# Optimization experiments

Measured on AMD Instinct MI355X. Metric: run time of the kernel, lower is better.

Reference implementation:

```python
import jax, jax.numpy as jnp
import numpy as np

B, L, E = 512, 64, 1024
D_MODEL, H = 1024, 16
HD = D_MODEL // H  # 64
SMOL_CH, SMOL_HID, SMOL_GEN = 32, 256, 256
LN_EPS = 1e-3


def _layernorm(x, g, b, eps=LN_EPS):
    m = jnp.mean(x, axis=-1, keepdims=True)
    v = jnp.mean(jnp.square(x - m), axis=-1, keepdims=True)
    return (x - m) * jax.lax.rsqrt(v + eps) * g + b


def setup_inputs() -> dict:
    key = jax.random.key(0)
    ks = jax.random.split(key, 12)
    s = lambda fan_in: 1.0 / np.sqrt(fan_in)
    inp = {
        'x': jax.random.normal(ks[0], (B, L, E), dtype=jnp.float32),
        # attention projections (stored as [in, out])
        'wq': jax.random.normal(ks[1], (E, D_MODEL), dtype=jnp.float32) * s(E),
        'bq': jnp.zeros((D_MODEL,), jnp.float32),
        'wk': jax.random.normal(ks[2], (E, D_MODEL), dtype=jnp.float32) * s(E),
        'bk': jnp.zeros((D_MODEL,), jnp.float32),
        'wv': jax.random.normal(ks[3], (E, D_MODEL), dtype=jnp.float32) * s(E),
        'bv': jnp.zeros((D_MODEL,), jnp.float32),
        'wo': jax.random.normal(ks[4], (D_MODEL, E), dtype=jnp.float32) * s(D_MODEL),
        'bo': jnp.zeros((E,), jnp.float32),
        # smolgen hypernetwork
        'sc_w': jax.random.normal(ks[5], (E, SMOL_CH), dtype=jnp.float32) * s(E),
        'sh1_w': jax.random.normal(ks[6], (L * SMOL_CH, SMOL_HID), dtype=jnp.float32) * s(L * SMOL_CH),
        'sh1_b': jnp.zeros((SMOL_HID,), jnp.float32),
        'ln1_g': jnp.ones((SMOL_HID,), jnp.float32),
        'ln1_b': jnp.zeros((SMOL_HID,), jnp.float32),
        'sg_w': jax.random.normal(ks[7], (SMOL_HID, H * SMOL_GEN), dtype=jnp.float32) * s(SMOL_HID),
        'sg_b': jnp.zeros((H * SMOL_GEN,), jnp.float32),
        'ln2_g': jnp.ones((H * SMOL_GEN,), jnp.float32),
        'ln2_b': jnp.zeros((H * SMOL_GEN,), jnp.float32),
        'swg_w': jax.random.normal(ks[8], (SMOL_GEN, L * L), dtype=jnp.float32) * s(SMOL_GEN),
    }
    return inp


def reference(x, wq, bq, wk, bk, wv, bv, wo, bo,
              sc_w, sh1_w, sh1_b, ln1_g, ln1_b,
              sg_w, sg_b, ln2_g, ln2_b, swg_w):
    b, l, _ = x.shape
    # q/k/v projections -> [b, h, l, hd]
    q = (x @ wq + bq).reshape(b, l, H, HD).transpose(0, 2, 1, 3)
    k = (x @ wk + bk).reshape(b, l, H, HD).transpose(0, 2, 1, 3)
    v = (x @ wv + bv).reshape(b, l, H, HD).transpose(0, 2, 1, 3)

    scale = jnp.sqrt(jnp.asarray(HD, x.dtype))
    attn_logits = jnp.einsum('bhqd,bhkd->bhqk', q, k) / scale  # [b,h,l,l]

    # smolgen: per-batch, per-head additive bias on the logits
    compressed = (x @ sc_w).reshape(b, l * SMOL_CH)            # [b, 2048]
    hidden = _layernorm(jax.nn.silu(compressed @ sh1_w + sh1_b), ln1_g, ln1_b)
    gen = _layernorm(jax.nn.silu(hidden @ sg_w + sg_b), ln2_g, ln2_b)
    gen = gen.reshape(b, H, SMOL_GEN)
    smol_w = (gen @ swg_w).reshape(b, H, l, l)
    attn_logits = attn_logits + smol_w

    # manual numerically-stable softmax (as in source)
    attn_logits = attn_logits - jnp.max(attn_logits, axis=-1, keepdims=True)
    attn_weights = jnp.exp(attn_logits)
    attn_weights = attn_weights / jnp.sum(attn_weights, axis=-1, keepdims=True)

    attn_output = jnp.einsum('bhqk,bhkd->bhqd', attn_weights, v)
    attn_output = attn_output.transpose(0, 2, 1, 3).reshape(b, l, D_MODEL)
    return attn_output @ wo + bo
```

## Files before the change

### kernel.cpp

```cpp
#include <hip/hip_runtime.h>
#include <hip/hip_bf16.h>

typedef unsigned short u16;
typedef __attribute__((ext_vector_type(8))) short short8;
typedef __attribute__((ext_vector_type(4))) float f32x4;
typedef const __attribute__((address_space(1))) void GV;
typedef __attribute__((address_space(3))) void LV;
#define GLOAD16(g, l) __builtin_amdgcn_global_load_lds((GV*)(g), (LV*)(l), 16, 0, 0)
#define BAR() asm volatile("s_barrier" ::: "memory")

#define BATCH 512
#define LSEQ  64
#define EMB   1024
#define NH    16
#define NQKV  3328
#define MROWS (BATCH*LSEQ)

__device__ __forceinline__ u16 f2b(float f){
  __hip_bfloat16 h = __float2bfloat16(f);
  return *reinterpret_cast<u16*>(&h);
}
__device__ __forceinline__ float b2f(u16 u){
  return __uint_as_float(((unsigned)u) << 16);
}

__global__ __launch_bounds__(256) void f32_to_bf16_v4(const float* __restrict__ src,
                                                      u16* __restrict__ dst){
  size_t i = ((size_t)blockIdx.x * 256 + threadIdx.x) * 4;
  float4 v = *(const float4*)&src[i];
  unsigned lo = (unsigned)f2b(v.x) | ((unsigned)f2b(v.y) << 16);
  unsigned hi = (unsigned)f2b(v.z) | ((unsigned)f2b(v.w) << 16);
  *(uint2*)&dst[i] = make_uint2(lo, hi);
}

__global__ __launch_bounds__(256) void transpose_to_bf16(const float* __restrict__ src,
                                                         u16* __restrict__ dst,
                                                         int K, int N, int dstLd, int dstRowOff){
  __shared__ float t[32][33];
  int nbx = N >> 5;
  int bx = blockIdx.x % nbx, by = blockIdx.x / nbx;
  int n0 = bx << 5, k0 = by << 5;
  int lx = threadIdx.x & 31, ly = threadIdx.x >> 5;
  #pragma unroll
  for (int i = 0; i < 32; i += 8)
    t[ly + i][lx] = src[(size_t)(k0 + ly + i) * N + n0 + lx];
  __syncthreads();
  #pragma unroll
  for (int i = 0; i < 32; i += 8)
    dst[(size_t)(dstRowOff + n0 + ly + i) * dstLd + k0 + lx] = f2b(t[lx][ly + i]);
}

__global__ __launch_bounds__(256) void build_qkv_bias(const float* __restrict__ bq,
                                                      const float* __restrict__ bk,
                                                      const float* __restrict__ bv,
                                                      float* __restrict__ out){
  int i = blockIdx.x * 256 + threadIdx.x;
  if (i < NQKV){
    float v = 0.f;
    if (i < 1024) v = bq[i];
    else if (i < 2048) v = bk[i - 1024];
    else if (i < 3072) v = bv[i - 2048];
    out[i] = v;
  }
}

template<int OUT_BF16, int HAS_BIAS>
__global__ __launch_bounds__(512, 2) void gemm256(const u16* __restrict__ A,
                                                  const u16* __restrict__ Bt,
                                                  const float* __restrict__ bias,
                                                  void* __restrict__ Cv,
                                                  int M, int N, int K){
  __shared__ u16 lA[2][16384];
  __shared__ u16 lB[2][16384];
  const int ntn = N >> 8;
  const int nwg = gridDim.x, bid = blockIdx.x;
  const int qq = nwg >> 3, r8 = nwg & 7, xcd = bid & 7, kk = bid >> 3;
  const int wg = (xcd < r8 ? xcd * (qq + 1) : r8 * (qq + 1) + (xcd - r8) * qq) + kk;
  const int tm = wg / ntn, tn = wg % ntn;
  const int m0 = tm << 8, n0 = tn << 8;
  const int tid = threadIdx.x;
  const int w = tid >> 6, lane = tid & 63;
  const int wm = w >> 2, wn = w & 3;
  const int l15 = lane & 15, l4 = lane >> 4;

  size_t ga[2][2], gb[2][2];
  #pragma unroll
  for (int j = 0; j < 2; j++){
    int ci = w * 128 + j * 64 + lane;
    int rh = ci >> 3, s = ci & 7;
    int gk = (s ^ (rh & 7)) * 8;
    #pragma unroll
    for (int h = 0; h < 2; h++){
      ga[h][j] = (size_t)(m0 + h * 128 + rh) * K + gk;
      gb[h][j] = (size_t)(n0 + h * 128 + rh) * K + gk;
    }
  }
  const int nk = K >> 6;

  auto stA = [&](int buf, int h, int kt){
    #pragma unroll
    for (int j = 0; j < 2; j++)
      GLOAD16(A + ga[h][j] + (size_t)kt * 64, &lA[buf][h * 8192 + (w * 128 + j * 64) * 8]);
  };
  auto stB = [&](int buf, int h, int kt){
    #pragma unroll
    for (int j = 0; j < 2; j++)
      GLOAD16(Bt + gb[h][j] + (size_t)kt * 64, &lB[buf][h * 8192 + (w * 128 + j * 64) * 8]);
  };

  stA(0, 0, 0); stB(0, 0, 0); stB(0, 1, 0); stA(0, 1, 0);
  stA(1, 0, 1); stB(1, 0, 1); stB(1, 1, 1);
  asm volatile("s_waitcnt vmcnt(6)" ::: "memory");
  BAR();

  f32x4 acc[8][4] = {};
  short8 a[4][2], b[4][2];

  for (int t = 0; t < nk; ++t){
    const int cur = t & 1;
    const u16* la = lA[cur];
    const u16* lb = lB[cur];

    #pragma unroll
    for (int f = 0; f < 4; f++){
      int r = f * 32 + wm * 16 + l15;
      #pragma unroll
      for (int ks = 0; ks < 2; ks++){
        int c = ks * 4 + l4;
        a[f][ks] = *(const short8*)&la[r * 64 + ((c ^ (r & 7)) * 8)];
      }
    }
    #pragma unroll
    for (int g = 0; g < 2; g++){
      int r = g * 64 + wn * 16 + l15;
      #pragma unroll
      for (int ks = 0; ks < 2; ks++){
        int c = ks * 4 + l4;
        b[g][ks] = *(const short8*)&lb[r * 64 + ((c ^ (r & 7)) * 8)];
      }
    }
    if (t + 1 < nk) stA(cur ^ 1, 1, t + 1);
    BAR();
    __builtin_amdgcn_s_setprio(1);
    #pragma unroll
    for (int f = 0; f < 4; f++)
      #pragma unroll
      for (int g = 0; g < 2; g++)
        #pragma unroll
        for (int ks = 0; ks < 2; ks++)
          acc[f][g] = __builtin_amdgcn_mfma_f32_16x16x32_bf16(a[f][ks], b[g][ks], acc[f][g], 0, 0, 0);
    __builtin_amdgcn_s_setprio(0);
    BAR();

    #pragma unroll
    for (int g = 2; g < 4; g++){
      int r = g * 64 + wn * 16 + l15;
      int rh = r & 127;
      #pragma unroll
      for (int ks = 0; ks < 2; ks++){
        int c = ks * 4 + l4;
        b[g][ks] = *(const short8*)&lb[8192 + rh * 64 + ((c ^ (rh & 7)) * 8)];
      }
    }
    if (t + 2 < nk) stA(cur, 0, t + 2);
    BAR();
    __builtin_amdgcn_s_setprio(1);
    #pragma unroll
    for (int f = 0; f < 4; f++)
      #pragma unroll
      for (int g = 2; g < 4; g++)
        #pragma unroll
        for (int ks = 0; ks < 2; ks++)
          acc[f][g] = __builtin_amdgcn_mfma_f32_16x16x32_bf16(a[f][ks], b[g][ks], acc[f][g], 0, 0, 0);
    __builtin_amdgcn_s_setprio(0);
    BAR();

    #pragma unroll
    for (int f = 0; f < 4; f++){
      int r = (f + 4) * 32 + wm * 16 + l15;
      int rh = r & 127;
      #pragma unroll
      for (int ks = 0; ks < 2; ks++){
        int c = ks * 4 + l4;
        a[f][ks] = *(const short8*)&la[8192 + rh * 64 + ((c ^ (rh & 7)) * 8)];
      }
    }
    if (t + 2 < nk) stB(cur, 0, t + 2);
    BAR();
    __builtin_amdgcn_s_setprio(1);
    #pragma unroll
    for (int f = 0; f < 4; f++)
      #pragma unroll
      for (int g = 2; g < 4; g++)
        #pragma unroll
        for (int ks = 0; ks < 2; ks++)
          acc[f + 4][g] = __builtin_amdgcn_mfma_f32_16x16x32_bf16(a[f][ks], b[g][ks], acc[f + 4][g], 0, 0, 0);
    __builtin_amdgcn_s_setprio(0);
    BAR();

    if (t + 2 < nk) stB(cur, 1, t + 2);
    if (t + 1 < nk){
      if (t + 2 < nk) asm volatile("s_waitcnt vmcnt(6)" ::: "memory");
      else            asm volatile("s_waitcnt vmcnt(0)" ::: "memory");
    }
    BAR();
    __builtin_amdgcn_s_setprio(1);
    #pragma unroll
    for (int f = 0; f < 4; f++)
      #pragma unroll
      for (int g = 0; g < 2; g++)
        #pragma unroll
        for (int ks = 0; ks < 2; ks++)
          acc[f + 4][g] = __builtin_amdgcn_mfma_f32_16x16x32_bf16(a[f][ks], b[g][ks], acc[f + 4][g], 0, 0, 0);
    __builtin_amdgcn_s_setprio(0);
    BAR();
  }

  #pragma unroll
  for (int f = 0; f < 8; f++){
    #pragma unroll
    for (int g = 0; g < 4; g++){
      int col = n0 + g * 64 + wn * 16 + l15;
      float bv = HAS_BIAS ? bias[col] : 0.0f;
      #pragma unroll
      for (int j = 0; j < 4; j++){
        int row = m0 + f * 32 + wm * 16 + l4 * 4 + j;
        float v = acc[f][g][j] + bv;
        if (OUT_BF16) ((u16*)Cv)[(size_t)row * N + col] = f2b(v);
        else          ((float*)Cv)[(size_t)row * N + col] = v;
      }
    }
  }
}

__device__ __forceinline__ float2 block_sum2(float a, float b, float* s, int tid){
  #pragma unroll
  for (int o = 32; o > 0; o >>= 1){ a += __shfl_down(a, o); b += __shfl_down(b, o); }
  int w = tid >> 6, lane = tid & 63;
  __syncthreads();
  if (lane == 0){ s[w * 2] = a; s[w * 2 + 1] = b; }
  __syncthreads();
  a = s[0] + s[2] + s[4] + s[6];
  b = s[1] + s[3] + s[5] + s[7];
  return make_float2(a, b);
}

__global__ __launch_bounds__(256) void smol_hidden(const u16* __restrict__ qkvb,
                                                   const float* __restrict__ sh1_w,
                                                   const float* __restrict__ sh1_b,
                                                   const float* __restrict__ ln1_g,
                                                   const float* __restrict__ ln1_b,
                                                   float* __restrict__ hidden){
  const int b0 = blockIdx.x * 2;
  const int tid = threadIdx.x;
  __shared__ u16 cb[2][2048];
  __shared__ float rs[8];
  #pragma unroll
  for (int bi = 0; bi < 2; bi++){
    int l = tid >> 2, cc = tid & 3;
    *(short8*)&cb[bi][tid * 8] =
        *(const short8*)&qkvb[(size_t)((b0 + bi) * 64 + l) * NQKV + 3072 + cc * 8];
  }
  __syncthreads();
  float acc0 = 0.f, acc1 = 0.f;
  for (int k8 = 0; k8 < 256; k8++){
    short8 c0 = *(const short8*)&cb[0][k8 * 8];
    short8 c1 = *(const short8*)&cb[1][k8 * 8];
    #pragma unroll
    for (int e = 0; e < 8; e++){
      float wv = sh1_w[(size_t)(k8 * 8 + e) * 256 + tid];
      acc0 += wv * b2f((u16)c0[e]);
      acc1 += wv * b2f((u16)c1[e]);
    }
  }
  float y0 = acc0 + sh1_b[tid]; y0 = y0 / (1.f + __expf(-y0));
  float y1 = acc1 + sh1_b[tid]; y1 = y1 / (1.f + __expf(-y1));
  float2 r0 = block_sum2(y0, y0 * y0, rs, tid);
  float2 r1 = block_sum2(y1, y1 * y1, rs, tid);
  float m0 = r0.x * (1.f / 256.f), v0 = r0.y * (1.f / 256.f) - m0 * m0;
  float m1 = r1.x * (1.f / 256.f), v1 = r1.y * (1.f / 256.f) - m1 * m1;
  hidden[(size_t)(b0    ) * 256 + tid] = (y0 - m0) * rsqrtf(v0 + 1e-3f) * ln1_g[tid] + ln1_b[tid];
  hidden[(size_t)(b0 + 1) * 256 + tid] = (y1 - m1) * rsqrtf(v1 + 1e-3f) * ln1_g[tid] + ln1_b[tid];
}

__global__ __launch_bounds__(256) void smol_gen(const float* __restrict__ hidden,
                                                const float* __restrict__ sg_w,
                                                const float* __restrict__ sg_b,
                                                const float* __restrict__ ln2_g,
                                                const float* __restrict__ ln2_b,
                                                u16* __restrict__ genb){
  const int b0 = blockIdx.x * 2;
  const int tid = threadIdx.x;
  __shared__ float hb[2][256];
  __shared__ float rs[8];
  hb[0][tid] = hidden[(size_t)b0 * 256 + tid];
  hb[1][tid] = hidden[(size_t)(b0 + 1) * 256 + tid];
  __syncthreads();
  float a0[16] = {}, a1[16] = {};
  for (int k = 0; k < 256; k++){
    float h0 = hb[0][k], h1 = hb[1][k];
    #pragma unroll
    for (int ci = 0; ci < 16; ci++){
      float wv = sg_w[(size_t)k * 4096 + ci * 256 + tid];
      a0[ci] += h0 * wv;
      a1[ci] += h1 * wv;
    }
  }
  float s0 = 0, q0 = 0, s1 = 0, q1 = 0;
  #pragma unroll
  for (int ci = 0; ci < 16; ci++){
    int col = ci * 256 + tid;
    float y = a0[ci] + sg_b[col]; y = y / (1.f + __expf(-y)); a0[ci] = y; s0 += y; q0 += y * y;
    y = a1[ci] + sg_b[col];       y = y / (1.f + __expf(-y)); a1[ci] = y; s1 += y; q1 += y * y;
  }
  float2 r0 = block_sum2(s0, q0, rs, tid);
  float2 r1 = block_sum2(s1, q1, rs, tid);
  float m0 = r0.x * (1.f / 4096.f), v0 = r0.y * (1.f / 4096.f) - m0 * m0;
  float m1 = r1.x * (1.f / 4096.f), v1 = r1.y * (1.f / 4096.f) - m1 * m1;
  float is0 = rsqrtf(v0 + 1e-3f), is1 = rsqrtf(v1 + 1e-3f);
  #pragma unroll
  for (int ci = 0; ci < 16; ci++){
    int col = ci * 256 + tid;
    genb[(size_t)(b0    ) * 4096 + col] = f2b((a0[ci] - m0) * is0 * ln2_g[col] + ln2_b[col]);
    genb[(size_t)(b0 + 1) * 4096 + col] = f2b((a1[ci] - m1) * is1 * ln2_g[col] + ln2_b[col]);
  }
}

__global__ __launch_bounds__(256) void attn_fused(const u16* __restrict__ qkvb,
                                                  const float* __restrict__ smol,
                                                  u16* __restrict__ aout){
  const int bh = blockIdx.x;
  const int b = bh >> 4, h = bh & 15;
  __shared__ u16 qs[4096], kts[4096], vts[4096], ps[4096];
  __shared__ float Ss[64 * 68];
  const int tid = threadIdx.x, w = tid >> 6, lane = tid & 63;
  const int wm = w >> 1, wn = w & 1;

  const u16* qb = qkvb + (size_t)(b * 64) * NQKV + h * 64;
  const u16* kb = qb + 1024;
  const u16* vb = qb + 2048;

  #pragma unroll
  for (int i = 0; i < 2; i++){
    int c = i * 256 + tid;
    int r = c >> 3, cc = c & 7;
    int pc = cc ^ (r & 7);
    *(short8*)&qs [r * 64 + pc * 8] = *(const short8*)&qb[(size_t)r * NQKV + cc * 8];
    *(short8*)&kts[r * 64 + pc * 8] = *(const short8*)&kb[(size_t)r * NQKV + cc * 8];
    short8 vv = *(const short8*)&vb[(size_t)r * NQKV + cc * 8];
    #pragma unroll
    for (int j = 0; j < 8; j++){
      int hd = cc * 8 + j;
      int pcv = (r >> 3) ^ (hd & 7);
      vts[hd * 64 + pcv * 8 + (r & 7)] = (u16)vv[j];
    }
  }
  __syncthreads();

  f32x4 sacc[2][2] = {};
  #pragma unroll
  for (int ksi = 0; ksi < 2; ksi++){
    short8 af[2], bfr[2];
    #pragma unroll
    for (int f = 0; f < 2; f++){
      int ra = wm * 32 + f * 16 + (lane & 15);
      int ca = ksi * 4 + (lane >> 4);
      af[f]  = *(const short8*)&qs [ra * 64 + (ca ^ (ra & 7)) * 8];
      int rb = wn * 32 + f * 16 + (lane & 15);
      bfr[f] = *(const short8*)&kts[rb * 64 + (ca ^ (rb & 7)) * 8];
    }
    #pragma unroll
    for (int fm = 0; fm < 2; fm++)
      #pragma unroll
      for (int fn = 0; fn < 2; fn++)
        sacc[fm][fn] = __builtin_amdgcn_mfma_f32_16x16x32_bf16(af[fm], bfr[fn], sacc[fm][fn], 0, 0, 0);
  }
  const float* sm = smol + (size_t)bh * 4096;
  #pragma unroll
  for (int fm = 0; fm < 2; fm++)
    #pragma unroll
    for (int fn = 0; fn < 2; fn++)
      #pragma unroll
      for (int j = 0; j < 4; j++){
        int q  = wm * 32 + fm * 16 + (lane >> 4) * 4 + j;
        int kp = wn * 32 + fn * 16 + (lane & 15);
        Ss[q * 68 + kp] = sacc[fm][fn][j] * 0.125f + sm[q * 64 + kp];
      }
  __syncthreads();

  {
    int row = w * 16 + (lane >> 2);
    int sub = lane & 3;
    float* srow = &Ss[row * 68];
    float vals[16];
    float mx = -3.4e38f;
    #pragma unroll
    for (int i = 0; i < 16; i++){ vals[i] = srow[sub * 16 + i]; mx = fmaxf(mx, vals[i]); }
    mx = fmaxf(mx, __shfl_xor(mx, 1));
    mx = fmaxf(mx, __shfl_xor(mx, 2));
    float s = 0.f;
    #pragma unroll
    for (int i = 0; i < 16; i++){ vals[i] = __expf(vals[i] - mx); s += vals[i]; }
    s += __shfl_xor(s, 1);
    s += __shfl_xor(s, 2);
    float rinv = 1.f / s;
    short8 o0, o1;
    #pragma unroll
    for (int i = 0; i < 8; i++){ o0[i] = (short)f2b(vals[i] * rinv); o1[i] = (short)f2b(vals[8 + i] * rinv); }
    int c0 = sub * 2, c1 = sub * 2 + 1;
    *(short8*)&ps[row * 64 + (c0 ^ (row & 7)) * 8] = o0;
    *(short8*)&ps[row * 64 + (c1 ^ (row & 7)) * 8] = o1;
  }
  __syncthreads();

  f32x4 oacc[2][2] = {};
  #pragma unroll
  for (int ksi = 0; ksi < 2; ksi++){
    short8 af[2], bfr[2];
    #pragma unroll
    for (int f = 0; f < 2; f++){
      int ra = wm * 32 + f * 16 + (lane & 15);
      int ca = ksi * 4 + (lane >> 4);
      af[f]  = *(const short8*)&ps [ra * 64 + (ca ^ (ra & 7)) * 8];
      int rb = wn * 32 + f * 16 + (lane & 15);
      bfr[f] = *(const short8*)&vts[rb * 64 + (ca ^ (rb & 7)) * 8];
    }
    #pragma unroll
    for (int fm = 0; fm < 2; fm++)
      #pragma unroll
      for (int fn = 0; fn < 2; fn++)
        oacc[fm][fn] = __builtin_amdgcn_mfma_f32_16x16x32_bf16(af[fm], bfr[fn], oacc[fm][fn], 0, 0, 0);
  }
  #pragma unroll
  for (int fm = 0; fm < 2; fm++)
    #pragma unroll
    for (int fn = 0; fn < 2; fn++)
      #pragma unroll
      for (int j = 0; j < 4; j++){
        int q  = wm * 32 + fm * 16 + (lane >> 4) * 4 + j;
        int hd = wn * 32 + fn * 16 + (lane & 15);
        aout[(size_t)(b * 64 + q) * 1024 + h * 64 + hd] = f2b(oacc[fm][fn][j]);
      }
}

extern "C" void kernel_launch(void* const* d_in, const int* in_sizes, int n_in,
                              void* d_out, int out_size, void* d_ws, size_t ws_size,
                              hipStream_t stream){
  const float* x     = (const float*)d_in[0];
  const float* wq    = (const float*)d_in[1];
  const float* bq    = (const float*)d_in[2];
  const float* wk    = (const float*)d_in[3];
  const float* bk    = (const float*)d_in[4];
  const float* wv    = (const float*)d_in[5];
  const float* bv    = (const float*)d_in[6];
  const float* wo    = (const float*)d_in[7];
  const float* bo    = (const float*)d_in[8];
  const float* sc_w  = (const float*)d_in[9];
  const float* sh1_w = (const float*)d_in[10];
  const float* sh1_b = (const float*)d_in[11];
  const float* ln1_g = (const float*)d_in[12];
  const float* ln1_b = (const float*)d_in[13];
  const float* sg_w  = (const float*)d_in[14];
  const float* sg_b  = (const float*)d_in[15];
  const float* ln2_g = (const float*)d_in[16];
  const float* ln2_b = (const float*)d_in[17];
  const float* swg_w = (const float*)d_in[18];

  char* ws = (char*)d_ws;
  size_t off = 0;
  auto alloc = [&](size_t bytes){ void* p = ws + off; off += (bytes + 255) & ~(size_t)255; return p; };
  u16*   xb    = (u16*)  alloc((size_t)MROWS * EMB * 2);
  u16*   wqkvT = (u16*)  alloc((size_t)NQKV * EMB * 2);
  float* qbias = (float*)alloc((size_t)NQKV * 4);
  u16*   woT   = (u16*)  alloc((size_t)1024 * 1024 * 2);
  u16*   swgT  = (u16*)  alloc((size_t)4096 * 256 * 2);
  u16*   qkvb  = (u16*)  alloc((size_t)MROWS * NQKV * 2);
  float* hid   = (float*)alloc((size_t)512 * 256 * 4);
  u16*   genb  = (u16*)  alloc((size_t)512 * 4096 * 2);
  float* smol  = (float*)alloc((size_t)8192 * 4096 * 4);
  u16*   aout  = (u16*)  alloc((size_t)MROWS * 1024 * 2);

  f32_to_bf16_v4<<<(MROWS * EMB) / 1024, 256, 0, stream>>>(x, xb);
  transpose_to_bf16<<<1024, 256, 0, stream>>>(wq,   wqkvT, 1024, 1024, 1024, 0);
  transpose_to_bf16<<<1024, 256, 0, stream>>>(wk,   wqkvT, 1024, 1024, 1024, 1024);
  transpose_to_bf16<<<1024, 256, 0, stream>>>(wv,   wqkvT, 1024, 1024, 1024, 2048);
  transpose_to_bf16<<<32,   256, 0, stream>>>(sc_w, wqkvT, 1024, 32,   1024, 3072);
  hipMemsetAsync(wqkvT + (size_t)3104 * 1024, 0, (size_t)(NQKV - 3104) * 1024 * 2, stream);
  transpose_to_bf16<<<1024, 256, 0, stream>>>(wo,    woT,  1024, 1024, 1024, 0);
  transpose_to_bf16<<<1024, 256, 0, stream>>>(swg_w, swgT, 256,  4096, 256,  0);
  build_qkv_bias<<<NQKV / 256, 256, 0, stream>>>(bq, bk, bv, qbias);

  gemm256<1, 1><<<(MROWS / 256) * (NQKV / 256), 512, 0, stream>>>(
      xb, wqkvT, qbias, qkvb, MROWS, NQKV, 1024);

  smol_hidden<<<BATCH / 2, 256, 0, stream>>>(qkvb, sh1_w, sh1_b, ln1_g, ln1_b, hid);
  smol_gen   <<<BATCH / 2, 256, 0, stream>>>(hid, sg_w, sg_b, ln2_g, ln2_b, genb);
  gemm256<0, 0><<<(8192 / 256) * (4096 / 256), 512, 0, stream>>>(
      genb, swgT, nullptr, smol, 8192, 4096, 256);

  attn_fused<<<BATCH * NH, 256, 0, stream>>>(qkvb, smol, aout);

  gemm256<0, 1><<<(MROWS / 256) * (1024 / 256), 512, 0, stream>>>(
      aout, woT, bo, d_out, MROWS, 1024, 1024);
}
```

Before: 942.9 us.

## Restructure GEMM fragment loads and vectorize smolgen kernels with 512 threads

The GEMM main loop now loads the first A half-tile into a separate register set for the next k-step right after the wait barrier, and loads all B fragments up front. That reorders LDS reads against the MFMA phases and cuts global address registers to two 32-bit offsets. The smol_hidden and smol_gen kernels move to 512-thread blocks: hidden splits K across 8 groups with float4 weight loads and a shared-memory partial reduction, and gen uses float4 weight loads and packed bf16 stores. These changes trade more live registers in the GEMM (an extra A fragment set) for better overlap. They also add extra LDS traffic in the small smolgen kernels. The 32-bit offsets could overflow for larger shapes.

```diff
diff --git a/kernel.cpp b/kernel.cpp
--- a/kernel.cpp
+++ b/kernel.cpp
@@ -23,14 +23,17 @@
 __device__ __forceinline__ float b2f(u16 u){
   return __uint_as_float(((unsigned)u) << 16);
 }
+__device__ __forceinline__ uint2 pack4(float4 v){
+  unsigned lo = (unsigned)f2b(v.x) | ((unsigned)f2b(v.y) << 16);
+  unsigned hi = (unsigned)f2b(v.z) | ((unsigned)f2b(v.w) << 16);
+  return make_uint2(lo, hi);
+}
 
 __global__ __launch_bounds__(256) void f32_to_bf16_v4(const float* __restrict__ src,
                                                       u16* __restrict__ dst){
   size_t i = ((size_t)blockIdx.x * 256 + threadIdx.x) * 4;
   float4 v = *(const float4*)&src[i];
-  unsigned lo = (unsigned)f2b(v.x) | ((unsigned)f2b(v.y) << 16);
-  unsigned hi = (unsigned)f2b(v.z) | ((unsigned)f2b(v.w) << 16);
-  *(uint2*)&dst[i] = make_uint2(lo, hi);
+  *(uint2*)&dst[i] = pack4(v);
 }
 
 __global__ __launch_bounds__(256) void transpose_to_bf16(const float* __restrict__ src,
@@ -83,38 +86,45 @@
   const int wm = w >> 2, wn = w & 3;
   const int l15 = lane & 15, l4 = lane >> 4;
 
-  size_t ga[2][2], gb[2][2];
-  #pragma unroll
-  for (int j = 0; j < 2; j++){
-    int ci = w * 128 + j * 64 + lane;
-    int rh = ci >> 3, s = ci & 7;
-    int gk = (s ^ (rh & 7)) * 8;
-    #pragma unroll
-    for (int h = 0; h < 2; h++){
-      ga[h][j] = (size_t)(m0 + h * 128 + rh) * K + gk;
-      gb[h][j] = (size_t)(n0 + h * 128 + rh) * K + gk;
-    }
-  }
-  const int nk = K >> 6;
+  const int ci = w * 128 + lane;
+  const int rh = ci >> 3, sl = ci & 7;
+  const int gk = (sl ^ (rh & 7)) * 8;
+  const unsigned aoff = (unsigned)((m0 + rh) * K + gk);
+  const unsigned boff = (unsigned)((n0 + rh) * K + gk);
 
   auto stA = [&](int buf, int h, int kt){
-    #pragma unroll
-    for (int j = 0; j < 2; j++)
-      GLOAD16(A + ga[h][j] + (size_t)kt * 64, &lA[buf][h * 8192 + (w * 128 + j * 64) * 8]);
+    const u16* p = A + aoff + (size_t)(h * 128) * K + (size_t)kt * 64;
+    GLOAD16(p,                &lA[buf][h * 8192 + (w * 128) * 8]);
+    GLOAD16(p + (size_t)8 * K, &lA[buf][h * 8192 + (w * 128 + 64) * 8]);
   };
   auto stB = [&](int buf, int h, int kt){
-    #pragma unroll
-    for (int j = 0; j < 2; j++)
-      GLOAD16(Bt + gb[h][j] + (size_t)kt * 64, &lB[buf][h * 8192 + (w * 128 + j * 64) * 8]);
+    const u16* p = Bt + boff + (size_t)(h * 128) * K + (size_t)kt * 64;
+    GLOAD16(p,                &lB[buf][h * 8192 + (w * 128) * 8]);
+    GLOAD16(p + (size_t)8 * K, &lB[buf][h * 8192 + (w * 128 + 64) * 8]);
   };
+
+  short8 a[4][2], a2[4][2], b[4][2];
+  auto read_a2 = [&](const u16* la){
+    #pragma unroll
+    for (int f = 0; f < 4; f++){
+      int r = f * 32 + wm * 16 + l15;
+      #pragma unroll
+      for (int ks = 0; ks < 2; ks++){
+        int c = ks * 4 + l4;
+        a2[f][ks] = *(const short8*)&la[r * 64 + ((c ^ (r & 7)) * 8)];
+      }
+    }
+  };
+
+  const int nk = K >> 6;
 
   stA(0, 0, 0); stB(0, 0, 0); stB(0, 1, 0); stA(0, 1, 0);
   stA(1, 0, 1); stB(1, 0, 1); stB(1, 1, 1);
   asm volatile("s_waitcnt vmcnt(6)" ::: "memory");
   BAR();
+  read_a2(lA[0]);
 
   f32x4 acc[8][4] = {};
-  short8 a[4][2], b[4][2];
 
   for (int t = 0; t < nk; ++t){
     const int cur = t & 1;
@@ -122,15 +132,6 @@
     const u16* lb = lB[cur];
 
     #pragma unroll
-    for (int f = 0; f < 4; f++){
-      int r = f * 32 + wm * 16 + l15;
-      #pragma unroll
-      for (int ks = 0; ks < 2; ks++){
-        int c = ks * 4 + l4;
-        a[f][ks] = *(const short8*)&la[r * 64 + ((c ^ (r & 7)) * 8)];
-      }
-    }
-    #pragma unroll
     for (int g = 0; g < 2; g++){
       int r = g * 64 + wn * 16 + l15;
       #pragma unroll
@@ -139,6 +140,15 @@
         b[g][ks] = *(const short8*)&lb[r * 64 + ((c ^ (r & 7)) * 8)];
       }
     }
+    #pragma unroll
+    for (int g = 2; g < 4; g++){
+      int r = (g - 2) * 64 + wn * 16 + l15;
+      #pragma unroll
+      for (int ks = 0; ks < 2; ks++){
+        int c = ks * 4 + l4;
+        b[g][ks] = *(const short8*)&lb[8192 + r * 64 + ((c ^ (r & 7)) * 8)];
+      }
+    }
     if (t + 1 < nk) stA(cur ^ 1, 1, t + 1);
     BAR();
     __builtin_amdgcn_s_setprio(1);
@@ -148,18 +158,17 @@
       for (int g = 0; g < 2; g++)
         #pragma unroll
         for (int ks = 0; ks < 2; ks++)
-          acc[f][g] = __builtin_amdgcn_mfma_f32_16x16x32_bf16(a[f][ks], b[g][ks], acc[f][g], 0, 0, 0);
+          acc[f][g] = __builtin_amdgcn_mfma_f32_16x16x32_bf16(a2[f][ks], b[g][ks], acc[f][g], 0, 0, 0);
     __builtin_amdgcn_s_setprio(0);
     BAR();
 
     #pragma unroll
-    for (int g = 2; g < 4; g++){
-      int r = g * 64 + wn * 16 + l15;
-      int rh = r & 127;
+    for (int f = 0; f < 4; f++){
+      int r = f * 32 + wm * 16 + l15;
       #pragma unroll
       for (int ks = 0; ks < 2; ks++){
         int c = ks * 4 + l4;
-        b[g][ks] = *(const short8*)&lb[8192 + rh * 64 + ((c ^ (rh & 7)) * 8)];
+        a[f][ks] = *(const short8*)&la[8192 + r * 64 + ((c ^ (r & 7)) * 8)];
       }
     }
     if (t + 2 < nk) stA(cur, 0, t + 2);
@@ -171,20 +180,10 @@
       for (int g = 2; g < 4; g++)
         #pragma unroll
         for (int ks = 0; ks < 2; ks++)
-          acc[f][g] = __builtin_amdgcn_mfma_f32_16x16x32_bf16(a[f][ks], b[g][ks], acc[f][g], 0, 0, 0);
+          acc[f][g] = __builtin_amdgcn_mfma_f32_16x16x32_bf16(a2[f][ks], b[g][ks], acc[f][g], 0, 0, 0);
     __builtin_amdgcn_s_setprio(0);
     BAR();
 
-    #pragma unroll
-    for (int f = 0; f < 4; f++){
-      int r = (f + 4) * 32 + wm * 16 + l15;
-      int rh = r & 127;
-      #pragma unroll
-      for (int ks = 0; ks < 2; ks++){
-        int c = ks * 4 + l4;
-        a[f][ks] = *(const short8*)&la[8192 + rh * 64 + ((c ^ (rh & 7)) * 8)];
-      }
-    }
     if (t + 2 < nk) stB(cur, 0, t + 2);
     BAR();
     __builtin_amdgcn_s_setprio(1);
@@ -204,6 +203,7 @@
       else            asm volatile("s_waitcnt vmcnt(0)" ::: "memory");
     }
     BAR();
+    if (t + 1 < nk) read_a2(lA[cur ^ 1]);
     __builtin_amdgcn_s_setprio(1);
     #pragma unroll
     for (int f = 0; f < 4; f++)
@@ -233,19 +233,7 @@
   }
 }
 
-__device__ __forceinline__ float2 block_sum2(float a, float b, float* s, int tid){
-  #pragma unroll
-  for (int o = 32; o > 0; o >>= 1){ a += __shfl_down(a, o); b += __shfl_down(b, o); }
-  int w = tid >> 6, lane = tid & 63;
-  __syncthreads();
-  if (lane == 0){ s[w * 2] = a; s[w * 2 + 1] = b; }
-  __syncthreads();
-  a = s[0] + s[2] + s[4] + s[6];
-  b = s[1] + s[3] + s[5] + s[7];
-  return make_float2(a, b);
-}
-
-__global__ __launch_bounds__(256) void smol_hidden(const u16* __restrict__ qkvb,
+__global__ __launch_bounds__(512) void smol_hidden(const u16* __restrict__ qkvb,
                                                    const float* __restrict__ sh1_w,
                                                    const float* __restrict__ sh1_b,
                                                    const float* __restrict__ ln1_g,
@@ -254,36 +242,48 @@
   const int b0 = blockIdx.x * 2;
   const int tid = threadIdx.x;
   __shared__ u16 cb[2][2048];
-  __shared__ float rs[8];
-  #pragma unroll
-  for (int bi = 0; bi < 2; bi++){
-    int l = tid >> 2, cc = tid & 3;
-    *(short8*)&cb[bi][tid * 8] =
+  __shared__ float part[8][2][256];
+  __shared__ float rs[16];
+  {
+    int bi = tid >> 8, rem = tid & 255;
+    int l = rem >> 2, cc = rem & 3;
+    *(short8*)&cb[bi][rem * 8] =
         *(const short8*)&qkvb[(size_t)((b0 + bi) * 64 + l) * NQKV + 3072 + cc * 8];
   }
   __syncthreads();
-  float acc0 = 0.f, acc1 = 0.f;
-  for (int k8 = 0; k8 < 256; k8++){
-    short8 c0 = *(const short8*)&cb[0][k8 * 8];
-    short8 c1 = *(const short8*)&cb[1][k8 * 8];
-    #pragma unroll
-    for (int e = 0; e < 8; e++){
-      float wv = sh1_w[(size_t)(k8 * 8 + e) * 256 + tid];
-      acc0 += wv * b2f((u16)c0[e]);
-      acc1 += wv * b2f((u16)c1[e]);
-    }
-  }
-  float y0 = acc0 + sh1_b[tid]; y0 = y0 / (1.f + __expf(-y0));
-  float y1 = acc1 + sh1_b[tid]; y1 = y1 / (1.f + __expf(-y1));
-  float2 r0 = block_sum2(y0, y0 * y0, rs, tid);
-  float2 r1 = block_sum2(y1, y1 * y1, rs, tid);
-  float m0 = r0.x * (1.f / 256.f), v0 = r0.y * (1.f / 256.f) - m0 * m0;
-  float m1 = r1.x * (1.f / 256.f), v1 = r1.y * (1.f / 256.f) - m1 * m1;
-  hidden[(size_t)(b0    ) * 256 + tid] = (y0 - m0) * rsqrtf(v0 + 1e-3f) * ln1_g[tid] + ln1_b[tid];
-  hidden[(size_t)(b0 + 1) * 256 + tid] = (y1 - m1) * rsqrtf(v1 + 1e-3f) * ln1_g[tid] + ln1_b[tid];
-}
-
-__global__ __launch_bounds__(256) void smol_gen(const float* __restrict__ hidden,
+  const int g = tid >> 6;
+  const int c4 = (tid & 63) * 4;
+  float4 a0 = {0,0,0,0}, a1 = {0,0,0,0};
+  for (int kk2 = 0; kk2 < 256; kk2++){
+    int k = g * 256 + kk2;
+    float4 wv = *(const float4*)&sh1_w[(size_t)k * 256 + c4];
+    float x0 = b2f(cb[0][k]), x1 = b2f(cb[1][k]);
+    a0.x += x0 * wv.x; a0.y += x0 * wv.y; a0.z += x0 * wv.z; a0.w += x0 * wv.w;
+    a1.x += x1 * wv.x; a1.y += x1 * wv.y; a1.z += x1 * wv.z; a1.w += x1 * wv.w;
+  }
+  *(float4*)&part[g][0][c4] = a0;
+  *(float4*)&part[g][1][c4] = a1;
+  __syncthreads();
+  const int bi = tid >> 8, col = tid & 255;
+  float y = sh1_b[col];
+  #pragma unroll
+  for (int g2 = 0; g2 < 8; g2++) y += part[g2][bi][col];
+  y = y / (1.f + __expf(-y));
+  float s = y, q = y * y;
+  #pragma unroll
+  for (int o = 32; o > 0; o >>= 1){ s += __shfl_down(s, o); q += __shfl_down(q, o); }
+  int wv_ = tid >> 6;
+  if ((tid & 63) == 0){ rs[wv_ * 2] = s; rs[wv_ * 2 + 1] = q; }
+  __syncthreads();
+  float S = 0, Q = 0;
+  #pragma unroll
+  for (int w2 = 0; w2 < 4; w2++){ S += rs[(bi * 4 + w2) * 2]; Q += rs[(bi * 4 + w2) * 2 + 1]; }
+  float m = S * (1.f / 256.f), var = Q * (1.f / 256.f) - m * m;
+  hidden[(size_t)(b0 + bi) * 256 + col] =
+      (y - m) * rsqrtf(var + 1e-3f) * ln1_g[col] + ln1_b[col];
+}
+
+__global__ __launch_bounds__(512) void smol_gen(const float* __restrict__ hidden,
                                                 const float* __restrict__ sg_w,
                                                 const float* __restrict__ sg_b,
                                                 const float* __restrict__ ln2_g,
@@ -292,38 +292,61 @@
   const int b0 = blockIdx.x * 2;
   const int tid = threadIdx.x;
   __shared__ float hb[2][256];
-  __shared__ float rs[8];
-  hb[0][tid] = hidden[(size_t)b0 * 256 + tid];
-  hb[1][tid] = hidden[(size_t)(b0 + 1) * 256 + tid];
-  __syncthreads();
-  float a0[16] = {}, a1[16] = {};
+  __shared__ float rs[32];
+  if (tid < 512) hb[tid >> 8][tid & 255] = hidden[(size_t)(b0 + (tid >> 8)) * 256 + (tid & 255)];
+  __syncthreads();
+  const int c4 = tid * 4;
+  float4 A00 = {0,0,0,0}, A01 = {0,0,0,0}, A10 = {0,0,0,0}, A11 = {0,0,0,0};
   for (int k = 0; k < 256; k++){
     float h0 = hb[0][k], h1 = hb[1][k];
-    #pragma unroll
-    for (int ci = 0; ci < 16; ci++){
-      float wv = sg_w[(size_t)k * 4096 + ci * 256 + tid];
-      a0[ci] += h0 * wv;
-      a1[ci] += h1 * wv;
-    }
-  }
+    float4 w0 = *(const float4*)&sg_w[(size_t)k * 4096 + c4];
+    float4 w1 = *(const float4*)&sg_w[(size_t)k * 4096 + 2048 + c4];
+    A00.x += h0 * w0.x; A00.y += h0 * w0.y; A00.z += h0 * w0.z; A00.w += h0 * w0.w;
+    A01.x += h0 * w1.x; A01.y += h0 * w1.y; A01.z += h0 * w1.z; A01.w += h0 * w1.w;
+    A10.x += h1 * w0.x; A10.y += h1 * w0.y; A10.z += h1 * w0.z; A10.w += h1 * w0.w;
+    A11.x += h1 * w1.x; A11.y += h1 * w1.y; A11.z += h1 * w1.z; A11.w += h1 * w1.w;
+  }
+  float4 b0v = *(const float4*)&sg_b[c4];
+  float4 b1v = *(const float4*)&sg_b[2048 + c4];
   float s0 = 0, q0 = 0, s1 = 0, q1 = 0;
-  #pragma unroll
-  for (int ci = 0; ci < 16; ci++){
-    int col = ci * 256 + tid;
-    float y = a0[ci] + sg_b[col]; y = y / (1.f + __expf(-y)); a0[ci] = y; s0 += y; q0 += y * y;
-    y = a1[ci] + sg_b[col];       y = y / (1.f + __expf(-y)); a1[ci] = y; s1 += y; q1 += y * y;
-  }
-  float2 r0 = block_sum2(s0, q0, rs, tid);
-  float2 r1 = block_sum2(s1, q1, rs, tid);
-  float m0 = r0.x * (1.f / 4096.f), v0 = r0.y * (1.f / 4096.f) - m0 * m0;
-  float m1 = r1.x * (1.f / 4096.f), v1 = r1.y * (1.f / 4096.f) - m1 * m1;
+  float* p;
+  #pragma unroll
+  for (int e = 0; e < 4; e++){
+    p = (float*)&A00; float y = p[e] + ((float*)&b0v)[e]; y = y / (1.f + __expf(-y)); p[e] = y; s0 += y; q0 += y * y;
+    p = (float*)&A01; y = p[e] + ((float*)&b1v)[e]; y = y / (1.f + __expf(-y)); p[e] = y; s0 += y; q0 += y * y;
+    p = (float*)&A10; y = p[e] + ((float*)&b0v)[e]; y = y / (1.f + __expf(-y)); p[e] = y; s1 += y; q1 += y * y;
+    p = (float*)&A11; y = p[e] + ((float*)&b1v)[e]; y = y / (1.f + __expf(-y)); p[e] = y; s1 += y; q1 += y * y;
+  }
+  #pragma unroll
+  for (int o = 32; o > 0; o >>= 1){
+    s0 += __shfl_down(s0, o); q0 += __shfl_down(q0, o);
+    s1 += __shfl_down(s1, o); q1 += __shfl_down(q1, o);
+  }
+  int wv_ = tid >> 6;
+  if ((tid & 63) == 0){ rs[wv_ * 4] = s0; rs[wv_ * 4 + 1] = q0; rs[wv_ * 4 + 2] = s1; rs[wv_ * 4 + 3] = q1; }
+  __syncthreads();
+  float S0 = 0, Q0 = 0, S1 = 0, Q1 = 0;
+  #pragma unroll
+  for (int w2 = 0; w2 < 8; w2++){
+    S0 += rs[w2 * 4]; Q0 += rs[w2 * 4 + 1]; S1 += rs[w2 * 4 + 2]; Q1 += rs[w2 * 4 + 3];
+  }
+  float m0 = S0 * (1.f / 4096.f), v0 = Q0 * (1.f / 4096.f) - m0 * m0;
+  float m1 = S1 * (1.f / 4096.f), v1 = Q1 * (1.f / 4096.f) - m1 * m1;
   float is0 = rsqrtf(v0 + 1e-3f), is1 = rsqrtf(v1 + 1e-3f);
-  #pragma unroll
-  for (int ci = 0; ci < 16; ci++){
-    int col = ci * 256 + tid;
-    genb[(size_t)(b0    ) * 4096 + col] = f2b((a0[ci] - m0) * is0 * ln2_g[col] + ln2_b[col]);
-    genb[(size_t)(b0 + 1) * 4096 + col] = f2b((a1[ci] - m1) * is1 * ln2_g[col] + ln2_b[col]);
-  }
+  float4 g0 = *(const float4*)&ln2_g[c4],        gb0 = *(const float4*)&ln2_b[c4];
+  float4 g1 = *(const float4*)&ln2_g[2048 + c4], gb1 = *(const float4*)&ln2_b[2048 + c4];
+  float4 o00, o01, o10, o11;
+  #pragma unroll
+  for (int e = 0; e < 4; e++){
+    ((float*)&o00)[e] = (((float*)&A00)[e] - m0) * is0 * ((float*)&g0)[e] + ((float*)&gb0)[e];
+    ((float*)&o01)[e] = (((float*)&A01)[e] - m0) * is0 * ((float*)&g1)[e] + ((float*)&gb1)[e];
+    ((float*)&o10)[e] = (((float*)&A10)[e] - m1) * is1 * ((float*)&g0)[e] + ((float*)&gb0)[e];
+    ((float*)&o11)[e] = (((float*)&A11)[e] - m1) * is1 * ((float*)&g1)[e] + ((float*)&gb1)[e];
+  }
+  *(uint2*)&genb[(size_t)(b0    ) * 4096 + c4]        = pack4(o00);
+  *(uint2*)&genb[(size_t)(b0    ) * 4096 + 2048 + c4] = pack4(o01);
+  *(uint2*)&genb[(size_t)(b0 + 1) * 4096 + c4]        = pack4(o10);
+  *(uint2*)&genb[(size_t)(b0 + 1) * 4096 + 2048 + c4] = pack4(o11);
 }
 
 __global__ __launch_bounds__(256) void attn_fused(const u16* __restrict__ qkvb,
@@ -493,8 +516,8 @@
   gemm256<1, 1><<<(MROWS / 256) * (NQKV / 256), 512, 0, stream>>>(
       xb, wqkvT, qbias, qkvb, MROWS, NQKV, 1024);
 
-  smol_hidden<<<BATCH / 2, 256, 0, stream>>>(qkvb, sh1_w, sh1_b, ln1_g, ln1_b, hid);
-  smol_gen   <<<BATCH / 2, 256, 0, stream>>>(hid, sg_w, sg_b, ln2_g, ln2_b, genb);
+  smol_hidden<<<BATCH / 2, 512, 0, stream>>>(qkvb, sh1_w, sh1_b, ln1_g, ln1_b, hid);
+  smol_gen   <<<BATCH / 2, 512, 0, stream>>>(hid, sg_w, sg_b, ln2_g, ln2_b, genb);
   gemm256<0, 0><<<(8192 / 256) * (4096 / 256), 512, 0, stream>>>(
       genb, swgT, nullptr, smol, 8192, 4096, 256);
 
```

Measured after the change: 900.8 us. -4.5%, faster.
